# Performance work log

Measured on AMD Instinct MI355X. Metric: run time of the kernel, lower is better.

The kernel has to match this reference:

```python
import jax, jax.numpy as jnp
import numpy as np

# Straight-through sign binarization (BinaryNet semantics: .data mutation => identity grad)
@jax.custom_vjp
def binarize(x):
    return jnp.sign(x)

def _bin_fwd(x):
    return jnp.sign(x), None

def _bin_bwd(res, g):
    return (g,)

binarize.defvjp(_bin_fwd, _bin_bwd)

def hardtanh(x):
    return jnp.clip(x, -1.0, 1.0)

def bconv2d(x, w, stride):
    # binarize both input and weight, VALID conv, NCHW/OIHW
    return jax.lax.conv_general_dilated(
        binarize(x), binarize(w),
        window_strides=(stride, stride), padding='VALID',
        dimension_numbers=('NCHW', 'OIHW', 'NCHW'))

def blinear(x, w):
    # binarize input and weight; w is [out, in]
    return binarize(x) @ binarize(w).T

def setup_inputs() -> dict:
    key = jax.random.key(0)
    ks = jax.random.split(key, 6)
    B = 131072
    return {
        'x':    jax.random.normal(ks[0], (B, 1, 15, 15), dtype=jnp.float32),
        'w1':   jax.random.normal(ks[1], (4, 1, 3, 3),  dtype=jnp.float32),
        'w2':   jax.random.normal(ks[2], (8, 4, 3, 3),  dtype=jnp.float32),
        'w3':   jax.random.normal(ks[3], (16, 8, 3, 3), dtype=jnp.float32),
        'wfc1': jax.random.normal(ks[4], (8, 16),       dtype=jnp.float32),
        'wfc2': jax.random.normal(ks[5], (1, 8),        dtype=jnp.float32),
    }

def reference(x, w1, w2, w3, wfc1, wfc2):
    out = hardtanh(bconv2d(x, w1, 2))        # [B,4,7,7]
    out = hardtanh(bconv2d(out, w2, 2))      # [B,8,3,3]
    out = hardtanh(bconv2d(out, w3, 2))      # [B,16,1,1]
    out = out.reshape(-1, 16)                # [B,16]
    out = hardtanh(blinear(out, wfc1))       # [B,8]
    out = blinear(out, wfc2)                 # [B,1]
    return out
```

## Files before the change

kernel.cpp:

```cpp
#include <hip/hip_runtime.h>
#include <stdint.h>

typedef uint32_t u32;
typedef uint64_t u64;


__global__ void prep_weights(const float* __restrict__ w1, const float* __restrict__ w2,
                             const float* __restrict__ w3, const float* __restrict__ wfc1,
                             const float* __restrict__ wfc2, u32* __restrict__ ws) {
  const int tid = threadIdx.x;
  if (tid < 81) ws[tid] = 0;
  __syncthreads();
  for (int i = tid; i < 1612; i += 1024) {
    if (i < 36) {
      const int c = i / 9, k = i % 9;
      if (w1[i] < 0.f) atomicOr(&ws[c], 1u << k);
    } else if (i < 324) {
      const int j = i - 36, d = j / 36, r = j % 36;
      const int c = r / 9, t = r % 9, ky = t / 3, kx = t % 3;
      const int bp = 12 * ky + 4 * kx + c;
      if (w2[j] < 0.f) atomicOr(&ws[8 + 2 * d + (bp >> 5)], 1u << (bp & 31));
    } else if (i < 1476) {
      const int j = i - 324, e = j / 72, r = j % 72;
      const int d = r / 9, t = r % 9, ky = t / 3, kx = t % 3;
      const int bp = 8 * (3 * ky + kx) + d;
      if (w3[j] < 0.f) {
        if (bp < 64) atomicOr(&ws[24 + 2 * e + (bp >> 5)], 1u << (bp & 31));
        else         atomicOr(&ws[56 + e], 1u << (bp - 64));
      }
    } else if (i < 1604) {
      const int j = i - 1476, row = j / 16, e = j % 16;
      if (wfc1[j] < 0.f) atomicOr(&ws[72 + row], 1u << e);
    } else {
      const int j = i - 1604;
      if (wfc2[j] < 0.f) atomicOr(&ws[80], 1u << j);
    }
  }
}

__global__ __launch_bounds__(64) void binnet(const float* __restrict__ x,
                                             const u32* __restrict__ ws,
                                             float* __restrict__ out) {
  __shared__ u64 st[228];
  const int lane = threadIdx.x;
  const int b0 = blockIdx.x * 64;

  const float* xw = x + (size_t)b0 * 225 + lane;
  if (lane < 3) st[225 + lane] = 0;
  #pragma unroll
  for (int g = 0; g < 5; ++g) {
    float v[45];
    #pragma unroll
    for (int k = 0; k < 45; ++k) v[k] = xw[(g * 45 + k) * 64];
    #pragma unroll
    for (int k = 0; k < 45; ++k) {
      const u64 m = __ballot(v[k] < 0.f);
      if (lane == 0) st[g * 45 + k] = m;
    }
  }
  __syncthreads();

  const u64* stw = st;
  const int f0 = 225 * lane;
  const int w0 = f0 >> 6;
  const int sh = f0 & 63;
  u64 Wd[5];
  #pragma unroll
  for (int i = 0; i < 5; ++i) Wd[i] = stw[w0 + i];
  u64 Bv[4];
  #pragma unroll
  for (int i = 0; i < 4; ++i)
    Bv[i] = (Wd[i] >> sh) | ((Wd[i + 1] << (63 - sh)) << 1);

  u32 rb[15];
  #pragma unroll
  for (int r = 0; r < 15; ++r) {
    const int f = 15 * r, w = f >> 6, o = f & 63;
    u64 v = Bv[w] >> o;
    if (o > 49) v |= Bv[w + 1] << (64 - o);
    rb[r] = (u32)v & 0x7FFFu;
  }

  const u32 w1p0 = ws[0], w1p1 = ws[1], w1p2 = ws[2], w1p3 = ws[3];
  u64 a1[4] = {0, 0, 0, 0};
  int pix = 0;
  #pragma unroll
  for (int oy = 0; oy < 7; ++oy) {
    const u32 r0 = rb[2 * oy], r1 = rb[2 * oy + 1], r2 = rb[2 * oy + 2];
    #pragma unroll
    for (int ox = 0; ox < 7; ++ox) {
      const u32 t9 = ((r0 >> (2 * ox)) & 7) | (((r1 >> (2 * ox)) & 7) << 3)
                   | (((r2 >> (2 * ox)) & 7) << 6);
      u32 nib = 0;
      nib |= (u32)(__popc(t9 ^ w1p0) >= 5) << 0;
      nib |= (u32)(__popc(t9 ^ w1p1) >= 5) << 1;
      nib |= (u32)(__popc(t9 ^ w1p2) >= 5) << 2;
      nib |= (u32)(__popc(t9 ^ w1p3) >= 5) << 3;
      a1[pix >> 4] |= (u64)nib << ((pix & 15) * 4);
      ++pix;
    }
  }

  const u64* w2qp = (const u64*)(ws + 8);
  u64 W2[8];
  #pragma unroll
  for (int d = 0; d < 8; ++d) W2[d] = w2qp[d];
  u64 v2lo = 0, nz2lo = 0; u32 v2hi = 0, nz2hi = 0;
  #pragma unroll
  for (int oy = 0; oy < 3; ++oy) {
    #pragma unroll
    for (int ox = 0; ox < 3; ++ox) {
      u64 T = 0;
      #pragma unroll
      for (int ky = 0; ky < 3; ++ky) {
        const int p = 4 * (7 * (2 * oy + ky) + 2 * ox);
        const int w = p >> 6, o = p & 63;
        u64 v = a1[w] >> o;
        if (o > 52) v |= a1[w + 1] << (64 - o);
        T |= (v & 0xFFFull) << (12 * ky);
      }
      const int pix2 = 3 * oy + ox;
      u32 bv = 0, bz = 0;
      #pragma unroll
      for (int d = 0; d < 8; ++d) {
        const int cnt = __popcll(T ^ W2[d]);
        bv |= (u32)(cnt > 18) << d;
        bz |= (u32)(cnt != 18) << d;
      }
      if (pix2 < 8) { v2lo |= (u64)bv << (8 * pix2); nz2lo |= (u64)bz << (8 * pix2); }
      else          { v2hi = bv; nz2hi = bz; }
    }
  }

  const u64* w3lo = (const u64*)(ws + 24);
  const u32* w3hi = ws + 56;
  u64 W3L[16]; u32 W3H[16];
  #pragma unroll
  for (int e = 0; e < 16; ++e) { W3L[e] = w3lo[e]; W3H[e] = w3hi[e]; }
  const int nztot = __popcll(nz2lo) + __popc(nz2hi);
  u32 s3v = 0, s3nz = 0;
  #pragma unroll
  for (int e = 0; e < 16; ++e) {
    const int cnt = __popcll(nz2lo & (v2lo ^ W3L[e])) + __popc(nz2hi & (v2hi ^ W3H[e]));
    const int s = nztot - 2 * cnt;
    s3v  |= (u32)(s < 0) << e;
    s3nz |= (u32)(s != 0) << e;
  }

  const u32* wf1 = ws + 72;
  u32 WF1[8];
  #pragma unroll
  for (int j = 0; j < 8; ++j) WF1[j] = wf1[j];
  const int n3 = __popc(s3nz);
  u32 hv = 0, hz = 0;
  #pragma unroll
  for (int j = 0; j < 8; ++j) {
    const int c2 = __popc(s3nz & (s3v ^ WF1[j]));
    const int s = n3 - 2 * c2;
    hv |= (u32)(s < 0) << j;
    hz |= (u32)(s != 0) << j;
  }

  const u32 wf2 = ws[80];
  const int c3 = __popc(hz & (hv ^ wf2));
  const int sfin = __popc(hz) - 2 * c3;
  out[b0 + lane] = (float)sfin;
}

extern "C" void kernel_launch(void* const* d_in, const int* in_sizes, int n_in,
                              void* d_out, int out_size, void* d_ws, size_t ws_size,
                              hipStream_t stream) {
  const float* x    = (const float*)d_in[0];
  const float* w1   = (const float*)d_in[1];
  const float* w2   = (const float*)d_in[2];
  const float* w3   = (const float*)d_in[3];
  const float* wfc1 = (const float*)d_in[4];
  const float* wfc2 = (const float*)d_in[5];
  u32* ws = (u32*)d_ws;
  float* out = (float*)d_out;
  const int B = in_sizes[0] / 225;

  prep_weights<<<1, 1024, 0, stream>>>(w1, w2, w3, wfc1, wfc2, ws);
  binnet<<<B / 64, 64, 0, stream>>>(x, ws, out);
}
```

Measured before the change: 190.0 us.

## Fuse weight binarization into main kernel via wavefront ballots

Drops the separate single-block weight-prep kernel and its atomics. Each wavefront now packs the binarized weights itself, using ballots over the float weights after loading its input tile. This removes a kernel launch and the serial dependency on prep, but every block re-reads about 1.6K weight floats and does extra ballots. Launch bounds also gain a minimum of 2 blocks per multiprocessor.

```diff
diff --git a/kernel.cpp b/kernel.cpp
--- a/kernel.cpp
+++ b/kernel.cpp
@@ -5,42 +5,13 @@
 typedef uint64_t u64;
 
 
-__global__ void prep_weights(const float* __restrict__ w1, const float* __restrict__ w2,
-                             const float* __restrict__ w3, const float* __restrict__ wfc1,
-                             const float* __restrict__ wfc2, u32* __restrict__ ws) {
-  const int tid = threadIdx.x;
-  if (tid < 81) ws[tid] = 0;
-  __syncthreads();
-  for (int i = tid; i < 1612; i += 1024) {
-    if (i < 36) {
-      const int c = i / 9, k = i % 9;
-      if (w1[i] < 0.f) atomicOr(&ws[c], 1u << k);
-    } else if (i < 324) {
-      const int j = i - 36, d = j / 36, r = j % 36;
-      const int c = r / 9, t = r % 9, ky = t / 3, kx = t % 3;
-      const int bp = 12 * ky + 4 * kx + c;
-      if (w2[j] < 0.f) atomicOr(&ws[8 + 2 * d + (bp >> 5)], 1u << (bp & 31));
-    } else if (i < 1476) {
-      const int j = i - 324, e = j / 72, r = j % 72;
-      const int d = r / 9, t = r % 9, ky = t / 3, kx = t % 3;
-      const int bp = 8 * (3 * ky + kx) + d;
-      if (w3[j] < 0.f) {
-        if (bp < 64) atomicOr(&ws[24 + 2 * e + (bp >> 5)], 1u << (bp & 31));
-        else         atomicOr(&ws[56 + e], 1u << (bp - 64));
-      }
-    } else if (i < 1604) {
-      const int j = i - 1476, row = j / 16, e = j % 16;
-      if (wfc1[j] < 0.f) atomicOr(&ws[72 + row], 1u << e);
-    } else {
-      const int j = i - 1604;
-      if (wfc2[j] < 0.f) atomicOr(&ws[80], 1u << j);
-    }
-  }
-}
-
-__global__ __launch_bounds__(64) void binnet(const float* __restrict__ x,
-                                             const u32* __restrict__ ws,
-                                             float* __restrict__ out) {
+__global__ __launch_bounds__(64, 2) void binnet(const float* __restrict__ x,
+                                                const float* __restrict__ w1,
+                                                const float* __restrict__ w2,
+                                                const float* __restrict__ w3,
+                                                const float* __restrict__ wfc1,
+                                                const float* __restrict__ wfc2,
+                                                float* __restrict__ out) {
   __shared__ u64 st[228];
   const int lane = threadIdx.x;
   const int b0 = blockIdx.x * 64;
@@ -58,12 +29,52 @@
       if (lane == 0) st[g * 45 + k] = m;
     }
   }
+
+  const float vw1 = w1[lane < 36 ? lane : 0];
+  const u64 m1 = __ballot((lane < 36) && (vw1 < 0.f));
+  const u32 w1p0 = (u32)(m1      ) & 0x1FFu;
+  const u32 w1p1 = (u32)(m1 >>  9) & 0x1FFu;
+  const u32 w1p2 = (u32)(m1 >> 18) & 0x1FFu;
+  const u32 w1p3 = (u32)(m1 >> 27) & 0x1FFu;
+
+  const int w2i = (lane < 36) ? ((lane & 3) * 9 + (lane >> 2)) : 0;
+  u64 W2[8];
+  #pragma unroll
+  for (int d = 0; d < 8; ++d) {
+    const float v = w2[d * 36 + w2i];
+    W2[d] = __ballot((lane < 36) && (v < 0.f));
+  }
+
+  const int w3i = (lane & 7) * 9 + (lane >> 3);
+  u64 W3L[16];
+  u32 W3H[16];
+  #pragma unroll
+  for (int e = 0; e < 16; ++e) W3L[e] = __ballot(w3[e * 72 + w3i] < 0.f);
+  {
+    const int hb = (lane & 7) * 9 + 8;
+    const u64 h0 = __ballot(w3[((lane >> 3)    ) * 72 + hb] < 0.f);
+    const u64 h1 = __ballot(w3[((lane >> 3) + 8) * 72 + hb] < 0.f);
+    #pragma unroll
+    for (int e = 0; e < 16; ++e)
+      W3H[e] = (u32)(((e < 8 ? h0 : h1) >> (8 * (e & 7))) & 0xFFu);
+  }
+
+  const u64 f0 = __ballot(wfc1[lane] < 0.f);
+  const u64 f1 = __ballot(wfc1[64 + lane] < 0.f);
+  u32 WF1[8];
+  #pragma unroll
+  for (int j = 0; j < 8; ++j)
+    WF1[j] = (u32)(((j < 4 ? f0 : f1) >> (16 * (j & 3))) & 0xFFFFu);
+
+  const float vf2 = wfc2[lane < 8 ? lane : 0];
+  const u32 wf2 = (u32)__ballot((lane < 8) && (vf2 < 0.f)) & 0xFFu;
+
   __syncthreads();
 
   const u64* stw = st;
-  const int f0 = 225 * lane;
-  const int w0 = f0 >> 6;
-  const int sh = f0 & 63;
+  const int f0i = 225 * lane;
+  const int w0 = f0i >> 6;
+  const int sh = f0i & 63;
   u64 Wd[5];
   #pragma unroll
   for (int i = 0; i < 5; ++i) Wd[i] = stw[w0 + i];
@@ -81,7 +92,6 @@
     rb[r] = (u32)v & 0x7FFFu;
   }
 
-  const u32 w1p0 = ws[0], w1p1 = ws[1], w1p2 = ws[2], w1p3 = ws[3];
   u64 a1[4] = {0, 0, 0, 0};
   int pix = 0;
   #pragma unroll
@@ -101,10 +111,6 @@
     }
   }
 
-  const u64* w2qp = (const u64*)(ws + 8);
-  u64 W2[8];
-  #pragma unroll
-  for (int d = 0; d < 8; ++d) W2[d] = w2qp[d];
   u64 v2lo = 0, nz2lo = 0; u32 v2hi = 0, nz2hi = 0;
   #pragma unroll
   for (int oy = 0; oy < 3; ++oy) {
@@ -132,11 +138,6 @@
     }
   }
 
-  const u64* w3lo = (const u64*)(ws + 24);
-  const u32* w3hi = ws + 56;
-  u64 W3L[16]; u32 W3H[16];
-  #pragma unroll
-  for (int e = 0; e < 16; ++e) { W3L[e] = w3lo[e]; W3H[e] = w3hi[e]; }
   const int nztot = __popcll(nz2lo) + __popc(nz2hi);
   u32 s3v = 0, s3nz = 0;
   #pragma unroll
@@ -147,10 +148,6 @@
     s3nz |= (u32)(s != 0) << e;
   }
 
-  const u32* wf1 = ws + 72;
-  u32 WF1[8];
-  #pragma unroll
-  for (int j = 0; j < 8; ++j) WF1[j] = wf1[j];
   const int n3 = __popc(s3nz);
   u32 hv = 0, hz = 0;
   #pragma unroll
@@ -161,7 +158,6 @@
     hz |= (u32)(s != 0) << j;
   }
 
-  const u32 wf2 = ws[80];
   const int c3 = __popc(hz & (hv ^ wf2));
   const int sfin = __popc(hz) - 2 * c3;
   out[b0 + lane] = (float)sfin;
@@ -176,10 +172,9 @@
   const float* w3   = (const float*)d_in[3];
   const float* wfc1 = (const float*)d_in[4];
   const float* wfc2 = (const float*)d_in[5];
-  u32* ws = (u32*)d_ws;
   float* out = (float*)d_out;
   const int B = in_sizes[0] / 225;
 
-  prep_weights<<<1, 1024, 0, stream>>>(w1, w2, w3, wfc1, wfc2, ws);
-  binnet<<<B / 64, 64, 0, stream>>>(x, ws, out);
+  (void)d_ws; (void)ws_size; (void)n_in; (void)out_size;
+  binnet<<<B / 64, 64, 0, stream>>>(x, w1, w2, w3, wfc1, wfc2, out);
 }
```

Result: faster. 185.5 us, median of 3 (-2.4%).
